# Performance work log

Hardware: AMD Instinct MI355X
Metric: run time of the kernel (lower is better)

The kernel has to match this reference:

```python
import jax, jax.numpy as jnp
import numpy as np

B, T, D, H = 8192, 64, 100, 110  # batch, t_grid_size, W_dim, 10+W_dim
S = T - 1                        # number of subnets / loop steps
SIG, R, DCOEF = 0.3, 0.1, 0.1
NUM_TIME_INTERVAL = 1.0
EPS = 1e-6


def setup_inputs() -> dict:
    key = jax.random.key(0)
    ks = jax.random.split(key, 16)
    f32 = jnp.float32
    inp = {
        "W": jax.random.normal(ks[0], (B, T, D), f32),
        "y_init": jax.random.uniform(ks[1], (1,), f32, 0.0, 1.0),
        "z_init": jax.random.uniform(ks[2], (1,), f32, -0.1, 0.1),
        # BatchNorm params: gamma ~ U(0.1,0.5), beta ~ N(0, 0.1) as in the keras initializers
        "g0": jax.random.uniform(ks[3], (S, D + 1), f32, 0.1, 0.5),
        "b0": 0.1 * jax.random.normal(ks[4], (S, D + 1), f32),
        "g1": jax.random.uniform(ks[5], (S, H), f32, 0.1, 0.5),
        "b1": 0.1 * jax.random.normal(ks[6], (S, H), f32),
        "g2": jax.random.uniform(ks[7], (S, H), f32, 0.1, 0.5),
        "b2": 0.1 * jax.random.normal(ks[8], (S, H), f32),
        "g3": jax.random.uniform(ks[9], (S, D), f32, 0.1, 0.5),
        "b3": 0.1 * jax.random.normal(ks[10], (S, D), f32),
        # Dense weights (glorot-ish scale); first two have no bias, last has bias
        "w0": jax.random.normal(ks[11], (S, D + 1, H), f32) / np.sqrt(D + 1),
        "w1": jax.random.normal(ks[12], (S, H, H), f32) / np.sqrt(H),
        "w2": jax.random.normal(ks[13], (S, H, D), f32) / np.sqrt(H),
        "bias2": jnp.zeros((S, D), f32),
    }
    return inp


def _bn(z, gamma, beta):
    # training-mode batch norm over batch axis (keras axis=1 -> per-feature)
    mu = jnp.mean(z, axis=0, keepdims=True)
    var = jnp.var(z, axis=0, keepdims=True)
    return gamma * (z - mu) * jax.lax.rsqrt(var + EPS) + beta


def reference(W, y_init, z_init, g0, b0, g1, b1, g2, b2, g3, b3, w0, w1, w2, bias2):
    delta_t = NUM_TIME_INTERVAL / T
    dW = jnp.transpose(W[:, 1:, :] - W[:, :-1, :], (1, 0, 2))  # [S, B, D]
    t_idx = jnp.arange(S, dtype=W.dtype)
    exp_coef = jnp.exp(-3.0 * R * (1.0 - t_idx * delta_t))      # [S]

    x0 = jnp.full((B, D), np.pi / 2, W.dtype)
    y0 = jnp.ones((B, 1), W.dtype) * y_init
    z0 = jnp.ones((B, D), W.dtype) * z_init

    def drift(x, y, ec):
        s = jnp.sum(jnp.sin(x), axis=1, keepdims=True)
        return -R * y + 0.5 * SIG ** 2 * ec * (DCOEF * s) ** 3

    def step(carry, xs):
        x, y, z = carry
        dw, ec, pg0, pb0, pg1, pb1, pg2, pb2, pg3, pb3, pw0, pw1, pw2, pbb = xs
        x = x + SIG * dw * y
        y = y - drift(x, y, ec) * delta_t + jnp.sum(z * dw, axis=1, keepdims=True)
        h = jnp.concatenate([x, y], axis=1)          # [B, D+1]
        h = _bn(h, pg0, pb0)
        h = jax.nn.relu(_bn(h @ pw0, pg1, pb1))      # [B, H]
        h = jax.nn.relu(_bn(h @ pw1, pg2, pb2))      # [B, H]
        z = _bn(h @ pw2 + pbb, pg3, pb3) / D         # [B, D]
        return (x, y, z), None

    xs = (dW, exp_coef, g0, b0, g1, b1, g2, b2, g3, b3, w0, w1, w2, bias2)
    (x, y, z), _ = jax.lax.scan(step, (x0, y0, z0), xs)

    # final step: Python loop leaves t = T-2; increment W[:,-1]-W[:,-2] == dW[-1]
    dw_last = dW[-1]
    x = x + SIG * y * dw_last
    y = y - drift(x, y, exp_coef[-1]) * delta_t + jnp.sum(z * dw_last, axis=1, keepdims=True)
    return (x, y)
```

## Files before the change

kernel.cpp:

```cpp
#include <hip/hip_runtime.h>
#include <cstdint>
#include <cstddef>

#define NBLK 128
#define NT   256
#define ROWS 64
#define DD   100
#define HH   110
#define NS   63
#define NGRP 16
#define GRP  (NBLK / NGRP)
#define REGF 512

typedef __bf16 bf16x8 __attribute__((ext_vector_type(8)));
typedef float  f32x16 __attribute__((ext_vector_type(16)));

struct Params {
  const float* W; const float* yini; const float* zini;
  const float* g0; const float* b0; const float* g1; const float* b1;
  const float* g2; const float* b2; const float* g3; const float* b3;
  const float* w0; const float* w1; const float* w2;
  float* out; float* slots; int* gcnt; int* scnt; int* rel;
};

__device__ __forceinline__ float agent_ld(const float* p_) {
  return __hip_atomic_load(p_, __ATOMIC_RELAXED, __HIP_MEMORY_SCOPE_AGENT);
}
__device__ __forceinline__ void agent_st(float* p_, float v) {
  __hip_atomic_store(p_, v, __ATOMIC_RELAXED, __HIP_MEMORY_SCOPE_AGENT);
}

__device__ __forceinline__ void sync_arrive(int* gcnt, int* scnt, int* rel, int bar) {
  asm volatile("s_waitcnt vmcnt(0)" ::: "memory");
  __syncthreads();
  if (threadIdx.x == 0) {
    int g = blockIdx.x & (NGRP - 1);
    int old = __hip_atomic_fetch_add(&gcnt[g * 16], 1,
                                     __ATOMIC_RELAXED, __HIP_MEMORY_SCOPE_AGENT);
    if (old == GRP * (bar + 1) - 1) {
      int so = __hip_atomic_fetch_add(scnt, 1,
                                      __ATOMIC_RELAXED, __HIP_MEMORY_SCOPE_AGENT);
      if (so == NGRP * (bar + 1) - 1) {
#pragma unroll
        for (int i = 0; i < NGRP; ++i)
          __hip_atomic_store(&rel[i * 16], bar + 1,
                             __ATOMIC_RELAXED, __HIP_MEMORY_SCOPE_AGENT);
      }
    }
  }
}
__device__ __forceinline__ void sync_wait(const int* rel, int bar) {
  if (threadIdx.x == 0) {
    while (__hip_atomic_load(&rel[(blockIdx.x & (NGRP - 1)) * 16],
                             __ATOMIC_RELAXED, __HIP_MEMORY_SCOPE_AGENT) < bar + 1)
      __builtin_amdgcn_s_sleep(1);
  }
  __syncthreads();
  asm volatile("" ::: "memory");
}

template<int K, int N>
__device__ __forceinline__ void issueB(const float* wg, int n, int half, float (*t)[8]) {
#pragma unroll
  for (int c = 0; c < 7; ++c) {
#pragma unroll
    for (int j = 0; j < 8; ++j) {
      int k = c * 16 + half * 8 + j;
      t[c][j] = (k < K && n < N) ? wg[k * N + n] : 0.f;
    }
  }
}

__device__ __forceinline__ void run_mfma2(const __bf16* hs, const float (*t)[8],
                                          int col, int half, f32x16* acc) {
  acc[0] = (f32x16)(0.f);
  acc[1] = (f32x16)(0.f);
#pragma unroll
  for (int c = 0; c < 7; ++c) {
    bf16x8 bfv;
#pragma unroll
    for (int j = 0; j < 8; ++j) bfv[j] = (__bf16)t[c][j];
    bf16x8 a0 = *(const bf16x8*)(hs + col * 120 + c * 16 + half * 8);
    bf16x8 a1 = *(const bf16x8*)(hs + (32 + col) * 120 + c * 16 + half * 8);
    acc[0] = __builtin_amdgcn_mfma_f32_32x32x16_bf16(a0, bfv, acc[0], 0, 0, 0);
    acc[1] = __builtin_amdgcn_mfma_f32_32x32x16_bf16(a1, bfv, acc[1], 0, 0, 0);
  }
}

__device__ __forceinline__ void frag2(const f32x16* acc, float* slot, int n, int N, int half) {
  float sm = 0.f, sq = 0.f;
#pragma unroll
  for (int m = 0; m < 2; ++m)
#pragma unroll
    for (int i = 0; i < 16; ++i) { float v = acc[m][i]; sm += v; sq += v * v; }
  sm += __shfl_xor(sm, 32);
  sq += __shfl_xor(sq, 32);
  if (half == 0 && n < N) {
    atomicAdd(&slot[n], sm);
    atomicAdd(&slot[112 + n], sq);
  }
}

__device__ __forceinline__ void frag3(const f32x16* acc, float* slot, int n, int half,
                                      const float* ysl) {
  float sm = 0.f, sq = 0.f, sy = 0.f;
#pragma unroll
  for (int m = 0; m < 2; ++m)
#pragma unroll
    for (int i = 0; i < 16; ++i) {
      float v = acc[m][i];
      int row = m * 32 + (i & 3) + 8 * (i >> 2) + 4 * half;
      sm += v; sq += v * v; sy += v * ysl[row];
    }
  sm += __shfl_xor(sm, 32);
  sq += __shfl_xor(sq, 32);
  sy += __shfl_xor(sy, 32);
  if (half == 0 && n < HH) {
    atomicAdd(&slot[n], sm);
    atomicAdd(&slot[112 + n], sq);
    atomicAdd(&slot[224 + n], sy);
  }
}

__device__ __forceinline__ void finalize2(const float* slot, const float* gam,
                                          const float* bet, int n, int N, float scale,
                                          float& a, float& c) {
  a = 0.f; c = 0.f;
  if (n < N) {
    float sm = agent_ld(&slot[n]);
    float sq = agent_ld(&slot[112 + n]);
    float mean = sm * (1.f / 8192.f);
    float var  = fmaxf(sq * (1.f / 8192.f) - mean * mean, 0.f);
    float au = gam[n] * rsqrtf(var + 1e-6f);
    a = au * scale;
    c = (bet[n] - mean * au) * scale;
  }
}

__device__ __forceinline__ void write_h(__bf16* hs, const f32x16* acc,
                                        float a, float c, int n, int half) {
  if (n < 112) {
#pragma unroll
    for (int m = 0; m < 2; ++m)
#pragma unroll
      for (int i = 0; i < 16; ++i) {
        int row = m * 32 + (i & 3) + 8 * (i >> 2) + 4 * half;
        float v = fmaxf(acc[m][i] * a + c, 0.f);
        hs[row * 120 + n] = (__bf16)v;
      }
  }
}

__device__ __forceinline__ void write_h1(__bf16* hs, const f32x16* acc,
                                         float a, float c, float ay, float cy,
                                         float w0yn, int n, int half, const float* ysl) {
  if (n < 112) {
#pragma unroll
    for (int m = 0; m < 2; ++m)
#pragma unroll
      for (int i = 0; i < 16; ++i) {
        int row = m * 32 + (i & 3) + 8 * (i >> 2) + 4 * half;
        float add = (ay * ysl[row] + cy) * w0yn;
        float v = fmaxf((acc[m][i] + add) * a + c, 0.f);
        hs[row * 120 + n] = (__bf16)v;
      }
  }
}

__device__ __forceinline__ void write_z(float* zsl, const f32x16* acc,
                                        float a, float c, int n, int half) {
  if (n < DD) {
#pragma unroll
    for (int m = 0; m < 2; ++m)
#pragma unroll
      for (int i = 0; i < 16; ++i) {
        int row = m * 32 + (i & 3) + 8 * (i >> 2) + 4 * half;
        zsl[row * 104 + n] = acc[m][i] * a + c;
      }
  }
}

__global__ __launch_bounds__(NT) void bsde_kernel(Params p) {
  __shared__ float xs[ROWS * 104];
  __shared__ float zs[ROWS * 104];
  __shared__ float dws[ROWS * 104];
  __shared__ float ys[ROWS];
  __shared__ float us[ROWS];
  __shared__ __bf16 hsb[ROWS * 120];
  __shared__ float aS[128], cS[128];
  __shared__ float syS[2];

  const int tid  = threadIdx.x;
  const int lane = tid & 63;
  const int wv   = tid >> 6;
  const int col  = lane & 31;
  const int half = lane >> 5;
  const int n    = wv * 32 + col;
  const int b0   = blockIdx.x * ROWS;

  {
    float z0 = p.zini[0];
    for (int i = tid; i < ROWS * 104; i += NT) { xs[i] = 1.57079632679f; zs[i] = z0; }
    for (int i = tid; i < ROWS * 120; i += NT) hsb[i] = (__bf16)0.f;
    if (tid < ROWS) ys[tid] = p.yini[0];
  }
  for (int idx = tid; idx < ROWS * 128; idx += NT) {
    int r = idx >> 7, d = idx & 127;
    if (d < DD) {
      const float* wr = p.W + (size_t)(b0 + r) * 6400 + d;
      dws[r * 104 + d] = wr[100] - wr[0];
    }
  }
  __syncthreads();

  int seg = 0;
  float tB[7][8];
  float w0yn;

  {
    int r = tid >> 2, l4 = tid & 3;
    float yr = ys[r];
    float ssum = 0.f;
#pragma unroll
    for (int i = 0; i < 25; ++i) {
      int d = l4 + 4 * i;
      float dw = dws[r * 104 + d];
      float xv = xs[r * 104 + d] + 0.3f * dw * yr;
      xs[r * 104 + d] = xv;
      ssum += __sinf(xv);
    }
    ssum += __shfl_down(ssum, 2, 4);
    ssum += __shfl_down(ssum, 1, 4);
    if (l4 == 0) {
      float ec = __expf(-0.3f);
      float tc = 0.1f * ssum;
      float drift = -0.1f * yr + 0.045f * ec * tc * tc * tc;
      us[r] = yr - drift * (1.f / 64.f);
    }
  }
  __syncthreads();
  {
    float* slot = p.slots + (seg % 3) * REGF;
    if (tid < DD) {
      float sm = 0.f, sq = 0.f;
      for (int r = 0; r < ROWS; ++r) { float v = xs[r * 104 + tid]; sm += v; sq += v * v; }
      atomicAdd(&slot[224 + tid], sm);
      atomicAdd(&slot[336 + tid], sq);
    }
    sync_arrive(p.gcnt, p.scnt, p.rel, seg);
    issueB<DD, HH>(p.w0, n, half, tB);
    w0yn = (n < HH) ? p.w0[100 * 110 + n] : 0.f;
    sync_wait(p.rel, seg);
    if (blockIdx.x < 2)
      agent_st(&p.slots[((seg + 2) % 3) * REGF + (int)blockIdx.x * 256 + tid], 0.f);
    if (tid < DD) {
      float sm = agent_ld(&slot[224 + tid]);
      float sq = agent_ld(&slot[336 + tid]);
      float mean = sm * (1.f / 8192.f);
      float var  = fmaxf(sq * (1.f / 8192.f) - mean * mean, 0.f);
      float au = p.g0[tid] * rsqrtf(var + 1e-6f);
      aS[tid] = au; cS[tid] = p.b0[tid] - mean * au;
    }
    ++seg;
  }
  __syncthreads();

  for (int s = 0; s < NS; ++s) {
    {
      int r = tid >> 2, l4 = tid & 3;
      float zdw = 0.f;
#pragma unroll
      for (int i = 0; i < 25; ++i) {
        int d = l4 + 4 * i;
        zdw += zs[r * 104 + d] * dws[r * 104 + d];
      }
      zdw += __shfl_down(zdw, 2, 4);
      zdw += __shfl_down(zdw, 1, 4);
      if (l4 == 0) ys[r] = us[r] + zdw;
    }
    __syncthreads();
    float* Eslot = p.slots + (seg % 3) * REGF;
    if (tid < 64) {
      float v = ys[tid], v2 = v * v;
#pragma unroll
      for (int off = 32; off > 0; off >>= 1) {
        v  += __shfl_down(v, off);
        v2 += __shfl_down(v2, off);
      }
      if (tid == 0) { atomicAdd(&Eslot[336], v); atomicAdd(&Eslot[337], v2); }
    }
    for (int idx = tid; idx < ROWS * 128; idx += NT) {
      int r = idx >> 7, d = idx & 127;
      if (d < DD) hsb[r * 120 + d] = (__bf16)(xs[r * 104 + d] * aS[d] + cS[d]);
    }
    __syncthreads();

    f32x16 acc[2];
    run_mfma2(hsb, tB, col, half, acc);
    frag3(acc, Eslot, n, half, ys);
    sync_arrive(p.gcnt, p.scnt, p.rel, seg);
    issueB<HH, HH>(p.w1 + (size_t)s * 12100, n, half, tB);
    sync_wait(p.rel, seg);
    if (blockIdx.x < 2)
      agent_st(&p.slots[((seg + 2) % 3) * REGF + (int)blockIdx.x * 256 + tid], 0.f);
    if (tid == 0) { syS[0] = agent_ld(&Eslot[336]); syS[1] = agent_ld(&Eslot[337]); }
    __syncthreads();
    float ay, cy, a1 = 0.f, c1 = 0.f;
    {
      float Sy  = syS[0];
      float Syy = syS[1];
      float my = Sy * (1.f / 8192.f);
      float vy = fmaxf(Syy * (1.f / 8192.f) - my * my, 0.f);
      float auy = p.g0[s * 101 + 100] * rsqrtf(vy + 1e-6f);
      ay = auy; cy = p.b0[s * 101 + 100] - my * auy;
      if (n < HH) {
        float G1 = agent_ld(&Eslot[n]);
        float G2 = agent_ld(&Eslot[112 + n]);
        float G3 = agent_ld(&Eslot[224 + n]);
        float Sv  = ay * Sy + 8192.f * cy;
        float Svv = ay * ay * Syy + 2.f * ay * cy * Sy + 8192.f * cy * cy;
        float w = w0yn;
        float S1 = G1 + w * Sv;
        float S2 = G2 + 2.f * w * (ay * G3 + cy * G1) + w * w * Svv;
        float mean = S1 * (1.f / 8192.f);
        float var  = fmaxf(S2 * (1.f / 8192.f) - mean * mean, 0.f);
        float au = p.g1[s * HH + n] * rsqrtf(var + 1e-6f);
        a1 = au; c1 = p.b1[s * HH + n] - mean * au;
      }
    }
    ++seg;
    write_h1(hsb, acc, a1, c1, ay, cy, w0yn, n, half, ys);
    __syncthreads();

    run_mfma2(hsb, tB, col, half, acc);
    float* Cslot = p.slots + (seg % 3) * REGF;
    frag2(acc, Cslot, n, HH, half);
    sync_arrive(p.gcnt, p.scnt, p.rel, seg);
    issueB<HH, DD>(p.w2 + (size_t)s * 11000, n, half, tB);
    if (s + 1 < NS) {
      for (int idx = tid; idx < ROWS * 128; idx += NT) {
        int r = idx >> 7, d = idx & 127;
        if (d < DD) {
          const float* wr = p.W + (size_t)(b0 + r) * 6400 + (s + 1) * 100 + d;
          dws[r * 104 + d] = wr[100] - wr[0];
        }
      }
      w0yn = (n < HH) ? p.w0[(size_t)(s + 1) * 11110 + 11000 + n] : 0.f;
    }
    sync_wait(p.rel, seg);
    if (blockIdx.x < 2)
      agent_st(&p.slots[((seg + 2) % 3) * REGF + (int)blockIdx.x * 256 + tid], 0.f);
    float a2, c2;
    finalize2(Cslot, p.g2 + s * HH, p.b2 + s * HH, n, HH, 1.f, a2, c2);
    ++seg;
    write_h(hsb, acc, a2, c2, n, half);
    __syncthreads();
    run_mfma2(hsb, tB, col, half, acc);
    float* Dslot = p.slots + (seg % 3) * REGF;
    frag2(acc, Dslot, n, DD, half);
    {
      int r = tid >> 2, l4 = tid & 3;
      float yr = ys[r];
      float ssum = 0.f;
#pragma unroll
      for (int i = 0; i < 25; ++i) {
        int d = l4 + 4 * i;
        float dw = dws[r * 104 + d];
        float xv = xs[r * 104 + d] + 0.3f * dw * yr;
        xs[r * 104 + d] = xv;
        ssum += __sinf(xv);
      }
      ssum += __shfl_down(ssum, 2, 4);
      ssum += __shfl_down(ssum, 1, 4);
      if (l4 == 0) {
        int ei = (s + 1 < NS) ? s + 1 : NS - 1;
        float ec = __expf(-0.3f * (1.f - (float)ei * (1.f / 64.f)));
        float tc = 0.1f * ssum;
        float drift = -0.1f * yr + 0.045f * ec * tc * tc * tc;
        us[r] = yr - drift * (1.f / 64.f);
      }
    }
    __syncthreads();
    if (tid < DD) {
      float sm = 0.f, sq = 0.f;
      for (int r = 0; r < ROWS; ++r) { float v = xs[r * 104 + tid]; sm += v; sq += v * v; }
      atomicAdd(&Dslot[224 + tid], sm);
      atomicAdd(&Dslot[336 + tid], sq);
    }
    sync_arrive(p.gcnt, p.scnt, p.rel, seg);
    if (s + 1 < NS) issueB<DD, HH>(p.w0 + (size_t)(s + 1) * 11110, n, half, tB);
    sync_wait(p.rel, seg);
    if (blockIdx.x < 2)
      agent_st(&p.slots[((seg + 2) % 3) * REGF + (int)blockIdx.x * 256 + tid], 0.f);
    float a3, c3;
    finalize2(Dslot, p.g3 + s * DD, p.b3 + s * DD, n, DD, 0.01f, a3, c3);
    if (s + 1 < NS && tid < DD) {
      float sm = agent_ld(&Dslot[224 + tid]);
      float sq = agent_ld(&Dslot[336 + tid]);
      float mean = sm * (1.f / 8192.f);
      float var  = fmaxf(sq * (1.f / 8192.f) - mean * mean, 0.f);
      float au = p.g0[(s + 1) * 101 + tid] * rsqrtf(var + 1e-6f);
      aS[tid] = au; cS[tid] = p.b0[(s + 1) * 101 + tid] - mean * au;
    }
    ++seg;
    write_z(zs, acc, a3, c3, n, half);
    __syncthreads();
  }

  {
    int r = tid >> 2, l4 = tid & 3;
    float zdw = 0.f;
#pragma unroll
    for (int i = 0; i < 25; ++i) {
      int d = l4 + 4 * i;
      zdw += zs[r * 104 + d] * dws[r * 104 + d];
    }
    zdw += __shfl_down(zdw, 2, 4);
    zdw += __shfl_down(zdw, 1, 4);
    if (l4 == 0) ys[r] = us[r] + zdw;
  }
  __syncthreads();

  for (int idx = tid; idx < ROWS * 128; idx += NT) {
    int r = idx >> 7, d = idx & 127;
    if (d < DD) p.out[(size_t)(b0 + r) * 100 + d] = xs[r * 104 + d];
  }
  if (tid < ROWS) p.out[819200 + b0 + tid] = ys[tid];
}

extern "C" void kernel_launch(void* const* d_in, const int* in_sizes, int n_in,
                              void* d_out, int out_size, void* d_ws, size_t ws_size,
                              hipStream_t stream) {
  Params p;
  p.W    = (const float*)d_in[0];
  p.yini = (const float*)d_in[1];
  p.zini = (const float*)d_in[2];
  p.g0   = (const float*)d_in[3];  p.b0 = (const float*)d_in[4];
  p.g1   = (const float*)d_in[5];  p.b1 = (const float*)d_in[6];
  p.g2   = (const float*)d_in[7];  p.b2 = (const float*)d_in[8];
  p.g3   = (const float*)d_in[9];  p.b3 = (const float*)d_in[10];
  p.w0   = (const float*)d_in[11]; p.w1 = (const float*)d_in[12];
  p.w2   = (const float*)d_in[13];
  p.out   = (float*)d_out;
  p.slots = (float*)d_ws;
  char* base = (char*)d_ws + (size_t)3 * REGF * 4;
  p.gcnt = (int*)base;
  p.scnt = (int*)(base + 1024);
  p.rel  = (int*)(base + 1088);

  size_t zbytes = (size_t)3 * REGF * 4 + 1024 + 64 + 1024;
  hipMemsetAsync(d_ws, 0, zbytes, stream);
  bsde_kernel<<<dim3(NBLK), dim3(NT), 0, stream>>>(p);
}
```

Before: 3.115 ms.

## Replace global atomic BN reductions with per-block slices and local slice sums

```diff
diff --git a/kernel.cpp b/kernel.cpp
--- a/kernel.cpp
+++ b/kernel.cpp
@@ -10,7 +10,8 @@
 #define NS   63
 #define NGRP 16
 #define GRP  (NBLK / NGRP)
-#define REGF 512
+#define NC2  272
+#define REG2 ((size_t)NBLK * NC2)
 
 typedef __bf16 bf16x8 __attribute__((ext_vector_type(8)));
 typedef float  f32x16 __attribute__((ext_vector_type(16)));
@@ -20,14 +21,19 @@
   const float* g0; const float* b0; const float* g1; const float* b1;
   const float* g2; const float* b2; const float* g3; const float* b3;
   const float* w0; const float* w1; const float* w2;
-  float* out; float* slots; int* gcnt; int* scnt; int* rel;
+  float* out; float2* slots; int* gcnt; int* scnt; int* rel;
 };
 
-__device__ __forceinline__ float agent_ld(const float* p_) {
-  return __hip_atomic_load(p_, __ATOMIC_RELAXED, __HIP_MEMORY_SCOPE_AGENT);
-}
-__device__ __forceinline__ void agent_st(float* p_, float v) {
-  __hip_atomic_store(p_, v, __ATOMIC_RELAXED, __HIP_MEMORY_SCOPE_AGENT);
+__device__ __forceinline__ void st2(float2* base, int chunk, float a, float b) {
+  union { float2 f; unsigned long long u; } v; v.f.x = a; v.f.y = b;
+  __hip_atomic_store((unsigned long long*)(base + chunk), v.u,
+                     __ATOMIC_RELAXED, __HIP_MEMORY_SCOPE_AGENT);
+}
+__device__ __forceinline__ float2 ld2(const float2* p_) {
+  union { float2 f; unsigned long long u; } v;
+  v.u = __hip_atomic_load((const unsigned long long*)p_, __ATOMIC_RELAXED,
+                          __HIP_MEMORY_SCOPE_AGENT);
+  return v.f;
 }
 
 __device__ __forceinline__ void sync_arrive(int* gcnt, int* scnt, int* rel, int bar) {
@@ -59,6 +65,37 @@
   asm volatile("" ::: "memory");
 }
 
+template<int CMAX>
+__device__ __forceinline__ void slice_sum(const float2* reg, float2 (*sum2)[NC2],
+                                          int tid) {
+  const int wv = tid >> 6, l = tid & 63;
+  constexpr int R = (CMAX + 63) / 64;
+  float2 acc[R];
+#pragma unroll
+  for (int r = 0; r < R; ++r) { acc[r].x = 0.f; acc[r].y = 0.f; }
+  const float2* sl = reg + (size_t)(wv * 32) * NC2;
+  for (int b = 0; b < 32; ++b, sl += NC2) {
+#pragma unroll
+    for (int r = 0; r < R; ++r) {
+      int c = r * 64 + l;
+      if (c < CMAX) { float2 v = ld2(sl + c); acc[r].x += v.x; acc[r].y += v.y; }
+    }
+  }
+#pragma unroll
+  for (int r = 0; r < R; ++r) {
+    int c = r * 64 + l;
+    if (c < CMAX) sum2[wv][c] = acc[r];
+  }
+  __syncthreads();
+  for (int c = tid; c < CMAX; c += NT) {
+    float2 a0 = sum2[0][c], a1 = sum2[1][c], a2 = sum2[2][c], a3 = sum2[3][c];
+    a0.x += a1.x + a2.x + a3.x;
+    a0.y += a1.y + a2.y + a3.y;
+    sum2[0][c] = a0;
+  }
+  __syncthreads();
+}
+
 template<int K, int N>
 __device__ __forceinline__ void issueB(const float* wg, int n, int half, float (*t)[8]) {
 #pragma unroll
@@ -87,7 +124,8 @@
   }
 }
 
-__device__ __forceinline__ void frag2(const f32x16* acc, float* slot, int n, int N, int half) {
+__device__ __forceinline__ void frag2_st(const f32x16* acc, float2* mysl,
+                                         int n, int N, int half) {
   float sm = 0.f, sq = 0.f;
 #pragma unroll
   for (int m = 0; m < 2; ++m)
@@ -95,14 +133,11 @@
     for (int i = 0; i < 16; ++i) { float v = acc[m][i]; sm += v; sq += v * v; }
   sm += __shfl_xor(sm, 32);
   sq += __shfl_xor(sq, 32);
-  if (half == 0 && n < N) {
-    atomicAdd(&slot[n], sm);
-    atomicAdd(&slot[112 + n], sq);
-  }
-}
-
-__device__ __forceinline__ void frag3(const f32x16* acc, float* slot, int n, int half,
-                                      const float* ysl) {
+  if (half == 0 && n < N) st2(mysl, n, sm, sq);
+}
+
+__device__ __forceinline__ void frag3_st(const f32x16* acc, float2* mysl,
+                                         int n, int half, const float* ysl) {
   float sm = 0.f, sq = 0.f, sy = 0.f;
 #pragma unroll
   for (int m = 0; m < 2; ++m)
@@ -115,25 +150,10 @@
   sm += __shfl_xor(sm, 32);
   sq += __shfl_xor(sq, 32);
   sy += __shfl_xor(sy, 32);
+  float syn = __shfl_down(sy, 1);
   if (half == 0 && n < HH) {
-    atomicAdd(&slot[n], sm);
-    atomicAdd(&slot[112 + n], sq);
-    atomicAdd(&slot[224 + n], sy);
-  }
-}
-
-__device__ __forceinline__ void finalize2(const float* slot, const float* gam,
-                                          const float* bet, int n, int N, float scale,
-                                          float& a, float& c) {
-  a = 0.f; c = 0.f;
-  if (n < N) {
-    float sm = agent_ld(&slot[n]);
-    float sq = agent_ld(&slot[112 + n]);
-    float mean = sm * (1.f / 8192.f);
-    float var  = fmaxf(sq * (1.f / 8192.f) - mean * mean, 0.f);
-    float au = gam[n] * rsqrtf(var + 1e-6f);
-    a = au * scale;
-    c = (bet[n] - mean * au) * scale;
+    st2(mysl, n, sm, sq);
+    if (!(n & 1)) st2(mysl, 112 + (n >> 1), sy, syn);
   }
 }
 
@@ -188,7 +208,7 @@
   __shared__ float us[ROWS];
   __shared__ __bf16 hsb[ROWS * 120];
   __shared__ float aS[128], cS[128];
-  __shared__ float syS[2];
+  __shared__ float2 sum2[4][NC2];
 
   const int tid  = threadIdx.x;
   const int lane = tid & 63;
@@ -240,22 +260,20 @@
   }
   __syncthreads();
   {
-    float* slot = p.slots + (seg % 3) * REGF;
+    float2* reg2 = p.slots + (seg & 1) * REG2;
+    float2* mysl = reg2 + (size_t)blockIdx.x * NC2;
     if (tid < DD) {
       float sm = 0.f, sq = 0.f;
       for (int r = 0; r < ROWS; ++r) { float v = xs[r * 104 + tid]; sm += v; sq += v * v; }
-      atomicAdd(&slot[224 + tid], sm);
-      atomicAdd(&slot[336 + tid], sq);
+      st2(mysl, 169 + tid, sm, sq);
     }
     sync_arrive(p.gcnt, p.scnt, p.rel, seg);
     issueB<DD, HH>(p.w0, n, half, tB);
     w0yn = (n < HH) ? p.w0[100 * 110 + n] : 0.f;
     sync_wait(p.rel, seg);
-    if (blockIdx.x < 2)
-      agent_st(&p.slots[((seg + 2) % 3) * REGF + (int)blockIdx.x * 256 + tid], 0.f);
+    slice_sum<269>(reg2, sum2, tid);
     if (tid < DD) {
-      float sm = agent_ld(&slot[224 + tid]);
-      float sq = agent_ld(&slot[336 + tid]);
+      float sm = sum2[0][169 + tid].x, sq = sum2[0][169 + tid].y;
       float mean = sm * (1.f / 8192.f);
       float var  = fmaxf(sq * (1.f / 8192.f) - mean * mean, 0.f);
       float au = p.g0[tid] * rsqrtf(var + 1e-6f);
@@ -279,7 +297,8 @@
       if (l4 == 0) ys[r] = us[r] + zdw;
     }
     __syncthreads();
-    float* Eslot = p.slots + (seg % 3) * REGF;
+    float2* Ereg = p.slots + (seg & 1) * REG2;
+    float2* Emy  = Ereg + (size_t)blockIdx.x * NC2;
     if (tid < 64) {
       float v = ys[tid], v2 = v * v;
 #pragma unroll
@@ -287,7 +306,7 @@
         v  += __shfl_down(v, off);
         v2 += __shfl_down(v2, off);
       }
-      if (tid == 0) { atomicAdd(&Eslot[336], v); atomicAdd(&Eslot[337], v2); }
+      if (tid == 0) st2(Emy, 168, v, v2);
     }
     for (int idx = tid; idx < ROWS * 128; idx += NT) {
       int r = idx >> 7, d = idx & 127;
@@ -297,26 +316,24 @@
 
     f32x16 acc[2];
     run_mfma2(hsb, tB, col, half, acc);
-    frag3(acc, Eslot, n, half, ys);
+    frag3_st(acc, Emy, n, half, ys);
     sync_arrive(p.gcnt, p.scnt, p.rel, seg);
     issueB<HH, HH>(p.w1 + (size_t)s * 12100, n, half, tB);
     sync_wait(p.rel, seg);
-    if (blockIdx.x < 2)
-      agent_st(&p.slots[((seg + 2) % 3) * REGF + (int)blockIdx.x * 256 + tid], 0.f);
-    if (tid == 0) { syS[0] = agent_ld(&Eslot[336]); syS[1] = agent_ld(&Eslot[337]); }
-    __syncthreads();
+    slice_sum<169>(Ereg, sum2, tid);
     float ay, cy, a1 = 0.f, c1 = 0.f;
     {
-      float Sy  = syS[0];
-      float Syy = syS[1];
+      float Sy  = sum2[0][168].x;
+      float Syy = sum2[0][168].y;
       float my = Sy * (1.f / 8192.f);
       float vy = fmaxf(Syy * (1.f / 8192.f) - my * my, 0.f);
       float auy = p.g0[s * 101 + 100] * rsqrtf(vy + 1e-6f);
       ay = auy; cy = p.b0[s * 101 + 100] - my * auy;
       if (n < HH) {
-        float G1 = agent_ld(&Eslot[n]);
-        float G2 = agent_ld(&Eslot[112 + n]);
-        float G3 = agent_ld(&Eslot[224 + n]);
+        float G1 = sum2[0][n].x;
+        float G2 = sum2[0][n].y;
+        float2 g3c = sum2[0][112 + (n >> 1)];
+        float G3 = (n & 1) ? g3c.y : g3c.x;
         float Sv  = ay * Sy + 8192.f * cy;
         float Svv = ay * ay * Syy + 2.f * ay * cy * Sy + 8192.f * cy * cy;
         float w = w0yn;
@@ -333,8 +350,8 @@
     __syncthreads();
 
     run_mfma2(hsb, tB, col, half, acc);
-    float* Cslot = p.slots + (seg % 3) * REGF;
-    frag2(acc, Cslot, n, HH, half);
+    float2* Creg = p.slots + (seg & 1) * REG2;
+    frag2_st(acc, Creg + (size_t)blockIdx.x * NC2, n, HH, half);
     sync_arrive(p.gcnt, p.scnt, p.rel, seg);
     issueB<HH, DD>(p.w2 + (size_t)s * 11000, n, half, tB);
     if (s + 1 < NS) {
@@ -348,16 +365,22 @@
       w0yn = (n < HH) ? p.w0[(size_t)(s + 1) * 11110 + 11000 + n] : 0.f;
     }
     sync_wait(p.rel, seg);
-    if (blockIdx.x < 2)
-      agent_st(&p.slots[((seg + 2) % 3) * REGF + (int)blockIdx.x * 256 + tid], 0.f);
-    float a2, c2;
-    finalize2(Cslot, p.g2 + s * HH, p.b2 + s * HH, n, HH, 1.f, a2, c2);
+    slice_sum<112>(Creg, sum2, tid);
+    float a2 = 0.f, c2 = 0.f;
+    if (n < HH) {
+      float sm = sum2[0][n].x, sq = sum2[0][n].y;
+      float mean = sm * (1.f / 8192.f);
+      float var  = fmaxf(sq * (1.f / 8192.f) - mean * mean, 0.f);
+      float au = p.g2[s * HH + n] * rsqrtf(var + 1e-6f);
+      a2 = au; c2 = p.b2[s * HH + n] - mean * au;
+    }
     ++seg;
     write_h(hsb, acc, a2, c2, n, half);
     __syncthreads();
     run_mfma2(hsb, tB, col, half, acc);
-    float* Dslot = p.slots + (seg % 3) * REGF;
-    frag2(acc, Dslot, n, DD, half);
+    float2* Dreg = p.slots + (seg & 1) * REG2;
+    float2* Dmy  = Dreg + (size_t)blockIdx.x * NC2;
+    frag2_st(acc, Dmy, n, DD, half);
     {
       int r = tid >> 2, l4 = tid & 3;
       float yr = ys[r];
@@ -384,19 +407,23 @@
     if (tid < DD) {
       float sm = 0.f, sq = 0.f;
       for (int r = 0; r < ROWS; ++r) { float v = xs[r * 104 + tid]; sm += v; sq += v * v; }
-      atomicAdd(&Dslot[224 + tid], sm);
-      atomicAdd(&Dslot[336 + tid], sq);
+      st2(Dmy, 169 + tid, sm, sq);
     }
     sync_arrive(p.gcnt, p.scnt, p.rel, seg);
     if (s + 1 < NS) issueB<DD, HH>(p.w0 + (size_t)(s + 1) * 11110, n, half, tB);
     sync_wait(p.rel, seg);
-    if (blockIdx.x < 2)
-      agent_st(&p.slots[((seg + 2) % 3) * REGF + (int)blockIdx.x * 256 + tid], 0.f);
-    float a3, c3;
-    finalize2(Dslot, p.g3 + s * DD, p.b3 + s * DD, n, DD, 0.01f, a3, c3);
+    slice_sum<269>(Dreg, sum2, tid);
+    float a3 = 0.f, c3 = 0.f;
+    if (n < DD) {
+      float sm = sum2[0][n].x, sq = sum2[0][n].y;
+      float mean = sm * (1.f / 8192.f);
+      float var  = fmaxf(sq * (1.f / 8192.f) - mean * mean, 0.f);
+      float au = p.g3[s * DD + n] * rsqrtf(var + 1e-6f);
+      a3 = au * 0.01f;
+      c3 = (p.b3[s * DD + n] - mean * au) * 0.01f;
+    }
     if (s + 1 < NS && tid < DD) {
-      float sm = agent_ld(&Dslot[224 + tid]);
-      float sq = agent_ld(&Dslot[336 + tid]);
+      float sm = sum2[0][169 + tid].x, sq = sum2[0][169 + tid].y;
       float mean = sm * (1.f / 8192.f);
       float var  = fmaxf(sq * (1.f / 8192.f) - mean * mean, 0.f);
       float au = p.g0[(s + 1) * 101 + tid] * rsqrtf(var + 1e-6f);
@@ -442,13 +469,13 @@
   p.w0   = (const float*)d_in[11]; p.w1 = (const float*)d_in[12];
   p.w2   = (const float*)d_in[13];
   p.out   = (float*)d_out;
-  p.slots = (float*)d_ws;
-  char* base = (char*)d_ws + (size_t)3 * REGF * 4;
+  p.slots = (float2*)d_ws;
+  size_t slice_bytes = (size_t)2 * REG2 * sizeof(float2);
+  char* base = (char*)d_ws + slice_bytes;
   p.gcnt = (int*)base;
   p.scnt = (int*)(base + 1024);
   p.rel  = (int*)(base + 1088);
 
-  size_t zbytes = (size_t)3 * REGF * 4 + 1024 + 64 + 1024;
-  hipMemsetAsync(d_ws, 0, zbytes, stream);
+  hipMemsetAsync(base, 0, 1024 + 64 + 1024, stream);
   bsde_kernel<<<dim3(NBLK), dim3(NT), 0, stream>>>(p);
 }
```

Measured after the change: 7.616 ms. 144% more time.
